# Optimization experiments

Hardware: AMD Instinct MI355X
Metric: run time of the kernel (lower is better)

Reference implementation:

```python
import jax, jax.numpy as jnp
import numpy as np

N_NODES = 50000
N_EDGES = 800000
D_IN = 256
D_HID = 256
D_OUT = 256
BN_EPS = 1e-5
NORM_EPS = 1e-12


def _glorot(key, out_dim, in_dim):
    a = np.sqrt(6.0 / (in_dim + out_dim)).astype(np.float32)
    return jax.random.uniform(key, (out_dim, in_dim), jnp.float32, -a, a)


def setup_inputs() -> dict:
    key = jax.random.key(0)
    ks = jax.random.split(key, 8)
    x = jax.random.normal(ks[0], (N_NODES, D_IN), jnp.float32)
    edge_index = jax.random.randint(ks[1], (2, N_EDGES), 0, N_NODES, dtype=jnp.int32)
    batch = jnp.zeros((N_NODES,), jnp.int32)
    return {
        "x": x,
        "W1_l": _glorot(ks[2], D_HID, D_IN),
        "b1_l": jnp.zeros((D_HID,), jnp.float32),
        "W1_r": _glorot(ks[3], D_HID, D_IN),
        "W2_l": _glorot(ks[4], D_OUT, D_HID),
        "b2_l": jnp.zeros((D_OUT,), jnp.float32),
        "W2_r": _glorot(ks[5], D_OUT, D_HID),
        "gamma1": jnp.ones((D_HID,), jnp.float32),
        "beta1": jnp.zeros((D_HID,), jnp.float32),
        "edge_index": edge_index,
        "batch": batch,
    }


def _sage_conv(x, W_l, b_l, W_r, src, dst, n_nodes):
    # PyG SAGEConv (aggr='mean'): out = lin_l(mean_j x_j) + lin_r(x)
    msgs = x[src]                                            # [E, d] gather
    s = jax.ops.segment_sum(msgs, dst, num_segments=n_nodes)  # [N, d] scatter-add
    cnt = jax.ops.segment_sum(jnp.ones((src.shape[0], 1), x.dtype), dst,
                              num_segments=n_nodes)
    agg = jnp.where(cnt > 0, s / jnp.maximum(cnt, 1.0), 0.0)
    return agg @ W_l.T + b_l + x @ W_r.T


def _batch_norm(h, gamma, beta):
    mu = jnp.mean(h, axis=0)
    var = jnp.mean((h - mu) ** 2, axis=0)  # biased, as torch train-mode BN
    return (h - mu) * jax.lax.rsqrt(var + BN_EPS) * gamma + beta


def _l2_normalize(h):
    n = jnp.linalg.norm(h, axis=-1, keepdims=True)
    return h / jnp.maximum(n, NORM_EPS)


def reference(x, W1_l, b1_l, W1_r, W2_l, b2_l, W2_r, gamma1, beta1,
              edge_index, batch):
    n = x.shape[0]
    src, dst = edge_index[0], edge_index[1]
    # layer 1: SAGEConv -> BN (train stats) -> ReLU (dropout = identity in eval)
    h = _sage_conv(x, W1_l, b1_l, W1_r, src, dst, n)
    h = jax.nn.relu(_batch_norm(h, gamma1, beta1))
    # layer 2: SAGEConv -> L2 normalize
    h = _sage_conv(h, W2_l, b2_l, W2_r, src, dst, n)
    node_emb = _l2_normalize(h)
    # global mean pool over batch ids (single graph here), then normalize
    gsum = jax.ops.segment_sum(node_emb, batch, num_segments=1)
    gcnt = jax.ops.segment_sum(jnp.ones((n, 1), node_emb.dtype), batch,
                               num_segments=1)
    graph_emb = _l2_normalize(gsum / jnp.maximum(gcnt, 1.0))
    return node_emb, graph_emb
```

## Files before the change

kernel.cpp:

```cpp
#include <hip/hip_runtime.h>
#include <math.h>

#define NN 50000
#define NE 800000
#define D  256
#define SCB 196

typedef unsigned short u16;
typedef __attribute__((ext_vector_type(8))) short short8;
typedef __attribute__((ext_vector_type(8))) unsigned short u16x8;
typedef __attribute__((ext_vector_type(4))) float f32x4;

__device__ __forceinline__ u16 f2b(float f) {
    unsigned u = __float_as_uint(f);
    return (u16)((u + 0x7FFFu + ((u >> 16) & 1u)) >> 16);
}
__device__ __forceinline__ float b2f(u16 b) {
    return __uint_as_float(((unsigned)b) << 16);
}

__device__ __forceinline__ void gl16(const u16* g, u16* l) {
    __builtin_amdgcn_global_load_lds(
        (const __attribute__((address_space(1))) void*)g,
        (__attribute__((address_space(3))) void*)l, 16, 0, 0);
}

__global__ void degree_kernel(const int* __restrict__ dst, int* __restrict__ deg) {
    int e = blockIdx.x * blockDim.x + threadIdx.x;
    if (e < NE) atomicAdd(&deg[dst[e]], 1);
}

__global__ void scanA_kernel(const int* __restrict__ deg, int* __restrict__ partial) {
    int t = threadIdx.x;
    int i = blockIdx.x * 256 + t;
    int v = (i < NN) ? deg[i] : 0;
#pragma unroll
    for (int o = 32; o; o >>= 1) v += __shfl_xor(v, o);
    __shared__ int sm[4];
    if ((t & 63) == 0) sm[t >> 6] = v;
    __syncthreads();
    if (t == 0) partial[blockIdx.x] = sm[0] + sm[1] + sm[2] + sm[3];
}

__global__ void scanB_kernel(const int* __restrict__ partial, int* __restrict__ base,
                             int* __restrict__ offs) {
    __shared__ int sm[256];
    int t = threadIdx.x;
    int v = (t < SCB) ? partial[t] : 0;
    sm[t] = v;
    __syncthreads();
    for (int off = 1; off < 256; off <<= 1) {
        int u = 0;
        if (t >= off) u = sm[t - off];
        __syncthreads();
        sm[t] += u;
        __syncthreads();
    }
    if (t < SCB) base[t] = sm[t] - v;
    if (t == 255) offs[NN] = sm[255];
}

__global__ void scanC_kernel(const int* __restrict__ deg, const int* __restrict__ base,
                             int* __restrict__ offs, int* __restrict__ cur) {
    __shared__ int sm[256];
    int t = threadIdx.x;
    int i = blockIdx.x * 256 + t;
    int v = (i < NN) ? deg[i] : 0;
    sm[t] = v;
    __syncthreads();
    for (int off = 1; off < 256; off <<= 1) {
        int u = 0;
        if (t >= off) u = sm[t - off];
        __syncthreads();
        sm[t] += u;
        __syncthreads();
    }
    int o = base[blockIdx.x] + sm[t] - v;
    if (i < NN) {
        offs[i] = o;
        cur[i] = o;
    }
}

__global__ void fill_kernel(const int* __restrict__ src, const int* __restrict__ dst,
                            int* __restrict__ cur, int* __restrict__ csr) {
    int e = blockIdx.x * blockDim.x + threadIdx.x;
    if (e < NE) {
        int pos = atomicAdd(&cur[dst[e]], 1);
        csr[pos] = src[e];
    }
}

__global__ void wconv_kernel(const float* __restrict__ W1l, const float* __restrict__ W1r,
                             const float* __restrict__ W2l, const float* __restrict__ W2r,
                             u16* __restrict__ Wcat1, u16* __restrict__ Wcat2) {
    int r = blockIdx.x;
    int j = threadIdx.x;
    Wcat1[r * 512 + j]       = f2b(W1l[r * 256 + j]);
    Wcat1[r * 512 + 256 + j] = f2b(W1r[r * 256 + j]);
    Wcat2[r * 512 + j]       = f2b(W2l[r * 256 + j]);
    Wcat2[r * 512 + 256 + j] = f2b(W2r[r * 256 + j]);
}

__global__ void xconv_kernel(const float* __restrict__ x, u16* __restrict__ Acat) {
    int idx = blockIdx.x * blockDim.x + threadIdx.x;
    int r = idx >> 6;
    int c4 = (idx & 63) * 4;
    float4 v = *(const float4*)&x[(size_t)r * 256 + c4];
    ushort4 o;
    o.x = f2b(v.x); o.y = f2b(v.y); o.z = f2b(v.z); o.w = f2b(v.w);
    *(ushort4*)&Acat[(size_t)r * 512 + 256 + c4] = o;
}

__global__ __launch_bounds__(256)
void agg_kernel(const u16* __restrict__ Acat, const int* __restrict__ csr,
                const int* __restrict__ offs, u16* __restrict__ AcatW) {
    int wid = (blockIdx.x * blockDim.x + threadIdx.x) >> 6;
    int lane = threadIdx.x & 63;
    if (wid >= NN) return;
    int beg = offs[wid];
    int end = offs[wid + 1];
    int deg = end - beg;
    int half = lane >> 5;
    int lc = (lane & 31) * 8;
    int mid = beg + ((deg + 1) >> 1);
    int e  = half ? mid : beg;
    int hi = half ? end : mid;
    float a[8] = {0.f, 0.f, 0.f, 0.f, 0.f, 0.f, 0.f, 0.f};
    for (; e + 3 < hi; e += 4) {
        int s0 = csr[e + 0];
        int s1 = csr[e + 1];
        int s2 = csr[e + 2];
        int s3 = csr[e + 3];
        u16x8 v0 = *(const u16x8*)&Acat[(size_t)s0 * 512 + 256 + lc];
        u16x8 v1 = *(const u16x8*)&Acat[(size_t)s1 * 512 + 256 + lc];
        u16x8 v2 = *(const u16x8*)&Acat[(size_t)s2 * 512 + 256 + lc];
        u16x8 v3 = *(const u16x8*)&Acat[(size_t)s3 * 512 + 256 + lc];
#pragma unroll
        for (int i = 0; i < 8; i++)
            a[i] += (b2f(v0[i]) + b2f(v1[i])) + (b2f(v2[i]) + b2f(v3[i]));
    }
    for (; e < hi; e++) {
        int s0 = csr[e];
        u16x8 v0 = *(const u16x8*)&Acat[(size_t)s0 * 512 + 256 + lc];
#pragma unroll
        for (int i = 0; i < 8; i++) a[i] += b2f(v0[i]);
    }
#pragma unroll
    for (int i = 0; i < 8; i++) a[i] += __shfl_xor(a[i], 32);
    float sc = (deg > 0) ? 1.0f / (float)deg : 0.0f;
    if (half == 0) {
        u16x8 o;
#pragma unroll
        for (int i = 0; i < 8; i++) o[i] = f2b(a[i] * sc);
        *(u16x8*)&AcatW[(size_t)wid * 512 + lc] = o;
    }
}

template<int BF16_OUT>
__global__ __launch_bounds__(256)
void mfma_gemm_kernel(const u16* __restrict__ A, const u16* __restrict__ W,
                      const float* __restrict__ bias, void* __restrict__ Cout) {
    __shared__ u16 As[4][128 * 32];
    __shared__ u16 Bs[4][128 * 32];
    const int tid = threadIdx.x;
    const int l = tid & 63;
    const int wid = tid >> 6;
    const int wr = wid >> 1, wc = wid & 1;
    const int row0 = blockIdx.x * 128;
    const int col0 = blockIdx.y * 128;

    const u16* aptr[2];
    const u16* bptr[2];
#pragma unroll
    for (int i = 0; i < 2; i++) {
        int row = wid * 32 + i * 16 + (l >> 2);
        int kg = (l & 3) ^ ((row >> 1) & 3);
        int ra = row0 + row;
        if (ra > NN - 1) ra = NN - 1;
        aptr[i] = A + (size_t)ra * 512 + kg * 8;
        bptr[i] = W + (size_t)(col0 + row) * 512 + kg * 8;
    }

    f32x4 acc[4][4] = {};

#define STAGE(b, t)                                                          \
    do {                                                                     \
        _Pragma("unroll") for (int i_ = 0; i_ < 2; i_++) {                   \
            u16* al = &As[b][(wid * 32 + i_ * 16) * 32];                     \
            u16* bl = &Bs[b][(wid * 32 + i_ * 16) * 32];                     \
            gl16(aptr[i_] + (t) * 32, al);                                   \
            gl16(bptr[i_] + (t) * 32, bl);                                   \
        }                                                                    \
    } while (0)

    STAGE(0, 0);
    STAGE(1, 1);

    const int kq = l >> 4;
    const int sw = ((l & 15) >> 1) & 3;
#pragma unroll
    for (int t = 0; t < 16; t++) {
        if (t + 2 < 16) STAGE((t + 2) & 3, t + 2);

        if (t < 14)       asm volatile("s_waitcnt vmcnt(8)" ::: "memory");
        else if (t == 14) asm volatile("s_waitcnt vmcnt(4)" ::: "memory");
        else              asm volatile("s_waitcnt vmcnt(0)" ::: "memory");
        __builtin_amdgcn_s_barrier();
        __builtin_amdgcn_sched_barrier(0);

        short8 af[4], bf[4];
#pragma unroll
        for (int m = 0; m < 4; m++) {
            int row = wr * 64 + m * 16 + (l & 15);
            af[m] = *(const short8*)&As[t & 3][row * 32 + (kq ^ sw) * 8];
        }
#pragma unroll
        for (int n = 0; n < 4; n++) {
            int row = wc * 64 + n * 16 + (l & 15);
            bf[n] = *(const short8*)&Bs[t & 3][row * 32 + (kq ^ sw) * 8];
        }
#pragma unroll
        for (int m = 0; m < 4; m++)
#pragma unroll
            for (int n = 0; n < 4; n++)
                acc[m][n] = __builtin_amdgcn_mfma_f32_16x16x32_bf16(
                    af[m], bf[n], acc[m][n], 0, 0, 0);
    }
#undef STAGE

    const int cq = l >> 4;
    const int cc = l & 15;
#pragma unroll
    for (int m = 0; m < 4; m++) {
#pragma unroll
        for (int n = 0; n < 4; n++) {
#pragma unroll
            for (int j = 0; j < 4; j++) {
                int r = row0 + wr * 64 + m * 16 + cq * 4 + j;
                int c = col0 + wc * 64 + n * 16 + cc;
                if (r < NN) {
                    float v = acc[m][n][j] + bias[c];
                    if (BF16_OUT)
                        ((u16*)Cout)[(size_t)r * 256 + c] = f2b(v);
                    else
                        ((float*)Cout)[(size_t)r * 256 + c] = v;
                }
            }
        }
    }
}

__global__ void colstats_kernel(const u16* __restrict__ h, float* __restrict__ stats) {
    int j = threadIdx.x;
    float s0 = 0.f, s1 = 0.f;
    for (int r = blockIdx.x; r < NN; r += gridDim.x) {
        float v = b2f(h[(size_t)r * 256 + j]);
        s0 += v;
        s1 += v * v;
    }
    atomicAdd(&stats[j], s0);
    atomicAdd(&stats[256 + j], s1);
}

__global__ void bnfin_kernel(const float* __restrict__ stats,
                             const float* __restrict__ gamma,
                             const float* __restrict__ beta,
                             float* __restrict__ scale,
                             float* __restrict__ shift) {
    int j = threadIdx.x;
    const float invN = 1.0f / (float)NN;
    float mu = stats[j] * invN;
    float var = stats[256 + j] * invN - mu * mu;
    float sc = gamma[j] * rsqrtf(var + 1e-5f);
    scale[j] = sc;
    shift[j] = beta[j] - mu * sc;
}

__global__ void bnrelu_kernel(const u16* __restrict__ hb,
                              const float* __restrict__ scale,
                              const float* __restrict__ shift,
                              u16* __restrict__ Acat) {
    int idx = blockIdx.x * blockDim.x + threadIdx.x;
    int r = idx >> 5;
    int c8 = (idx & 31) * 8;
    u16x8 v = *(const u16x8*)&hb[(size_t)r * 256 + c8];
    u16x8 o;
#pragma unroll
    for (int i = 0; i < 8; i++) {
        float f = b2f(v[i]) * scale[c8 + i] + shift[c8 + i];
        o[i] = f2b(fmaxf(f, 0.f));
    }
    *(u16x8*)&Acat[(size_t)r * 512 + 256 + c8] = o;
}

__global__ __launch_bounds__(512)
void l2norm_kernel(float* __restrict__ out, float* __restrict__ gsum) {
    __shared__ float sm[8 * 256];
    int wave = threadIdx.x >> 6;
    int lane = threadIdx.x & 63;
    float c0 = 0.f, c1 = 0.f, c2 = 0.f, c3 = 0.f;
    for (int r = blockIdx.x * 8 + wave; r < NN; r += gridDim.x * 8) {
        float4 v = *(float4*)&out[(size_t)r * 256 + lane * 4];
        float sq = v.x * v.x + v.y * v.y + v.z * v.z + v.w * v.w;
#pragma unroll
        for (int o = 32; o; o >>= 1) sq += __shfl_xor(sq, o);
        float invn = 1.0f / fmaxf(sqrtf(sq), 1e-12f);
        v.x *= invn; v.y *= invn; v.z *= invn; v.w *= invn;
        *(float4*)&out[(size_t)r * 256 + lane * 4] = v;
        c0 += v.x; c1 += v.y; c2 += v.z; c3 += v.w;
    }
    *(float4*)&sm[wave * 256 + lane * 4] = make_float4(c0, c1, c2, c3);
    __syncthreads();
    int t = threadIdx.x;
    if (t < 256) {
        float s = 0.f;
#pragma unroll
        for (int w = 0; w < 8; w++) s += sm[w * 256 + t];
        atomicAdd(&gsum[t], s);
    }
}

__global__ void graph_kernel(const float* __restrict__ gsum, float* __restrict__ gout) {
    __shared__ float wsum[4];
    int j = threadIdx.x;
    float v = gsum[j] * (1.0f / (float)NN);
    float sq = v * v;
#pragma unroll
    for (int o = 32; o; o >>= 1) sq += __shfl_xor(sq, o);
    if ((j & 63) == 0) wsum[j >> 6] = sq;
    __syncthreads();
    float tot = wsum[0] + wsum[1] + wsum[2] + wsum[3];
    gout[j] = v / fmaxf(sqrtf(tot), 1e-12f);
}

extern "C" void kernel_launch(void* const* d_in, const int* in_sizes, int n_in,
                              void* d_out, int out_size, void* d_ws, size_t ws_size,
                              hipStream_t stream) {
    const float* x      = (const float*)d_in[0];
    const float* W1_l   = (const float*)d_in[1];
    const float* b1_l   = (const float*)d_in[2];
    const float* W1_r   = (const float*)d_in[3];
    const float* W2_l   = (const float*)d_in[4];
    const float* b2_l   = (const float*)d_in[5];
    const float* W2_r   = (const float*)d_in[6];
    const float* gamma1 = (const float*)d_in[7];
    const float* beta1  = (const float*)d_in[8];
    const int*   eidx   = (const int*)d_in[9];
    const int* src = eidx;
    const int* dst = eidx + NE;

    char* wsb = (char*)d_ws;
    int*   deg   = (int*)(wsb + 0);
    int*   offs  = (int*)(wsb + 200000);
    int*   cur   = (int*)(wsb + 400004);
    int*   csr   = (int*)(wsb + 600004);
    int*   part  = (int*)(wsb + 3800064);
    int*   base  = (int*)(wsb + 3801088);
    float* stats = (float*)(wsb + 3802112);
    float* gsum  = (float*)(wsb + 3804160);
    float* scale = (float*)(wsb + 3805184);
    float* shift = (float*)(wsb + 3806208);
    u16*   Wcat1 = (u16*)(wsb + 3807232);
    u16*   Wcat2 = (u16*)(wsb + 4069376);
    u16*   hb    = (u16*)(wsb + 4331520);
    u16*   Acat  = (u16*)(wsb + 29931520);
    float* out   = (float*)d_out;
    float* gout  = out + (size_t)NN * 256;

    hipMemsetAsync(deg, 0, NN * sizeof(int), stream);
    hipMemsetAsync(stats, 0, 3072, stream);

    wconv_kernel<<<256, 256, 0, stream>>>(W1_l, W1_r, W2_l, W2_r, Wcat1, Wcat2);
    xconv_kernel<<<12500, 256, 0, stream>>>(x, Acat);

    degree_kernel<<<(NE + 255) / 256, 256, 0, stream>>>(dst, deg);
    scanA_kernel<<<SCB, 256, 0, stream>>>(deg, part);
    scanB_kernel<<<1, 256, 0, stream>>>(part, base, offs);
    scanC_kernel<<<SCB, 256, 0, stream>>>(deg, base, offs, cur);
    fill_kernel<<<(NE + 255) / 256, 256, 0, stream>>>(src, dst, cur, csr);

    dim3 ggrid((NN + 127) / 128, 2);

    agg_kernel<<<12500, 256, 0, stream>>>(Acat, csr, offs, Acat);
    mfma_gemm_kernel<1><<<ggrid, 256, 0, stream>>>(Acat, Wcat1, b1_l, hb);
    colstats_kernel<<<512, 256, 0, stream>>>(hb, stats);
    bnfin_kernel<<<1, 256, 0, stream>>>(stats, gamma1, beta1, scale, shift);
    bnrelu_kernel<<<6250, 256, 0, stream>>>(hb, scale, shift, Acat);

    agg_kernel<<<12500, 256, 0, stream>>>(Acat, csr, offs, Acat);
    mfma_gemm_kernel<0><<<ggrid, 256, 0, stream>>>(Acat, Wcat2, b2_l, out);

    l2norm_kernel<<<1024, 512, 0, stream>>>(out, gsum);
    graph_kernel<<<1, 256, 0, stream>>>(gsum, gout);
}
```

Baseline: 395.4 us.

## Fuse BN column stats into GEMM epilogue, vectorize CSR build, unroll aggregation

Removes the separate column-statistics pass over the hidden activations by accumulating per-column sum and sum-of-squares in the first GEMM's epilogue, reducing across lanes with shuffles and committing with atomics. The degree and CSR-fill kernels now process four edges per thread with int4 loads. The aggregation loop is unrolled to eight neighbours so more gathers are in flight. The trade-offs are more atomics from GEMM blocks and higher register pressure in aggregation. Stats are now taken on the fp32 values before bf16 rounding, which shifts numerics slightly.

```diff
diff --git a/kernel.cpp b/kernel.cpp
--- a/kernel.cpp
+++ b/kernel.cpp
@@ -26,8 +26,16 @@
 }
 
 __global__ void degree_kernel(const int* __restrict__ dst, int* __restrict__ deg) {
-    int e = blockIdx.x * blockDim.x + threadIdx.x;
-    if (e < NE) atomicAdd(&deg[dst[e]], 1);
+    int e0 = (blockIdx.x * blockDim.x + threadIdx.x) * 4;
+    if (e0 + 3 < NE) {
+        int4 d = *(const int4*)&dst[e0];
+        atomicAdd(&deg[d.x], 1);
+        atomicAdd(&deg[d.y], 1);
+        atomicAdd(&deg[d.z], 1);
+        atomicAdd(&deg[d.w], 1);
+    } else {
+        for (int e = e0; e < NE; e++) atomicAdd(&deg[dst[e]], 1);
+    }
 }
 
 __global__ void scanA_kernel(const int* __restrict__ deg, int* __restrict__ partial) {
@@ -84,10 +92,23 @@
 
 __global__ void fill_kernel(const int* __restrict__ src, const int* __restrict__ dst,
                             int* __restrict__ cur, int* __restrict__ csr) {
-    int e = blockIdx.x * blockDim.x + threadIdx.x;
-    if (e < NE) {
-        int pos = atomicAdd(&cur[dst[e]], 1);
-        csr[pos] = src[e];
+    int e0 = (blockIdx.x * blockDim.x + threadIdx.x) * 4;
+    if (e0 + 3 < NE) {
+        int4 d = *(const int4*)&dst[e0];
+        int4 s = *(const int4*)&src[e0];
+        int p0 = atomicAdd(&cur[d.x], 1);
+        int p1 = atomicAdd(&cur[d.y], 1);
+        int p2 = atomicAdd(&cur[d.z], 1);
+        int p3 = atomicAdd(&cur[d.w], 1);
+        csr[p0] = s.x;
+        csr[p1] = s.y;
+        csr[p2] = s.z;
+        csr[p3] = s.w;
+    } else {
+        for (int e = e0; e < NE; e++) {
+            int pos = atomicAdd(&cur[dst[e]], 1);
+            csr[pos] = src[e];
+        }
     }
 }
 
@@ -127,15 +148,28 @@
     int e  = half ? mid : beg;
     int hi = half ? end : mid;
     float a[8] = {0.f, 0.f, 0.f, 0.f, 0.f, 0.f, 0.f, 0.f};
-    for (; e + 3 < hi; e += 4) {
-        int s0 = csr[e + 0];
-        int s1 = csr[e + 1];
-        int s2 = csr[e + 2];
-        int s3 = csr[e + 3];
+    for (; e + 7 < hi; e += 8) {
+        int s0 = csr[e + 0], s1 = csr[e + 1], s2 = csr[e + 2], s3 = csr[e + 3];
+        int s4 = csr[e + 4], s5 = csr[e + 5], s6 = csr[e + 6], s7 = csr[e + 7];
         u16x8 v0 = *(const u16x8*)&Acat[(size_t)s0 * 512 + 256 + lc];
         u16x8 v1 = *(const u16x8*)&Acat[(size_t)s1 * 512 + 256 + lc];
         u16x8 v2 = *(const u16x8*)&Acat[(size_t)s2 * 512 + 256 + lc];
         u16x8 v3 = *(const u16x8*)&Acat[(size_t)s3 * 512 + 256 + lc];
+        u16x8 v4 = *(const u16x8*)&Acat[(size_t)s4 * 512 + 256 + lc];
+        u16x8 v5 = *(const u16x8*)&Acat[(size_t)s5 * 512 + 256 + lc];
+        u16x8 v6 = *(const u16x8*)&Acat[(size_t)s6 * 512 + 256 + lc];
+        u16x8 v7 = *(const u16x8*)&Acat[(size_t)s7 * 512 + 256 + lc];
+#pragma unroll
+        for (int i = 0; i < 8; i++)
+            a[i] += ((b2f(v0[i]) + b2f(v1[i])) + (b2f(v2[i]) + b2f(v3[i]))) +
+                    ((b2f(v4[i]) + b2f(v5[i])) + (b2f(v6[i]) + b2f(v7[i])));
+    }
+    for (; e + 3 < hi; e += 4) {
+        int s0 = csr[e + 0], s1 = csr[e + 1], s2 = csr[e + 2], s3 = csr[e + 3];
+        u16x8 v0 = *(const u16x8*)&Acat[(size_t)s0 * 512 + 256 + lc];
+        u16x8 v1 = *(const u16x8*)&Acat[(size_t)s1 * 512 + 256 + lc];
+        u16x8 v2 = *(const u16x8*)&Acat[(size_t)s2 * 512 + 256 + lc];
+        u16x8 v3 = *(const u16x8*)&Acat[(size_t)s3 * 512 + 256 + lc];
 #pragma unroll
         for (int i = 0; i < 8; i++)
             a[i] += (b2f(v0[i]) + b2f(v1[i])) + (b2f(v2[i]) + b2f(v3[i]));
@@ -157,10 +191,11 @@
     }
 }
 
-template<int BF16_OUT>
+template<int BF16_OUT, int STATS>
 __global__ __launch_bounds__(256)
 void mfma_gemm_kernel(const u16* __restrict__ A, const u16* __restrict__ W,
-                      const float* __restrict__ bias, void* __restrict__ Cout) {
+                      const float* __restrict__ bias, void* __restrict__ Cout,
+                      float* __restrict__ stats) {
     __shared__ u16 As[4][128 * 32];
     __shared__ u16 Bs[4][128 * 32];
     const int tid = threadIdx.x;
@@ -232,35 +267,33 @@
     const int cq = l >> 4;
     const int cc = l & 15;
 #pragma unroll
-    for (int m = 0; m < 4; m++) {
-#pragma unroll
-        for (int n = 0; n < 4; n++) {
+    for (int n = 0; n < 4; n++) {
+        int c = col0 + wc * 64 + n * 16 + cc;
+        float t0 = 0.f, t1 = 0.f;
+#pragma unroll
+        for (int m = 0; m < 4; m++) {
 #pragma unroll
             for (int j = 0; j < 4; j++) {
                 int r = row0 + wr * 64 + m * 16 + cq * 4 + j;
-                int c = col0 + wc * 64 + n * 16 + cc;
                 if (r < NN) {
                     float v = acc[m][n][j] + bias[c];
                     if (BF16_OUT)
                         ((u16*)Cout)[(size_t)r * 256 + c] = f2b(v);
                     else
                         ((float*)Cout)[(size_t)r * 256 + c] = v;
+                    if (STATS) { t0 += v; t1 += v * v; }
                 }
             }
         }
-    }
-}
-
-__global__ void colstats_kernel(const u16* __restrict__ h, float* __restrict__ stats) {
-    int j = threadIdx.x;
-    float s0 = 0.f, s1 = 0.f;
-    for (int r = blockIdx.x; r < NN; r += gridDim.x) {
-        float v = b2f(h[(size_t)r * 256 + j]);
-        s0 += v;
-        s1 += v * v;
-    }
-    atomicAdd(&stats[j], s0);
-    atomicAdd(&stats[256 + j], s1);
+        if (STATS) {
+            t0 += __shfl_xor(t0, 16); t1 += __shfl_xor(t1, 16);
+            t0 += __shfl_xor(t0, 32); t1 += __shfl_xor(t1, 32);
+            if (cq == 0) {
+                atomicAdd(&stats[c], t0);
+                atomicAdd(&stats[256 + c], t1);
+            }
+        }
+    }
 }
 
 __global__ void bnfin_kernel(const float* __restrict__ stats,
@@ -374,22 +407,21 @@
     wconv_kernel<<<256, 256, 0, stream>>>(W1_l, W1_r, W2_l, W2_r, Wcat1, Wcat2);
     xconv_kernel<<<12500, 256, 0, stream>>>(x, Acat);
 
-    degree_kernel<<<(NE + 255) / 256, 256, 0, stream>>>(dst, deg);
+    degree_kernel<<<(NE / 4 + 255) / 256, 256, 0, stream>>>(dst, deg);
     scanA_kernel<<<SCB, 256, 0, stream>>>(deg, part);
     scanB_kernel<<<1, 256, 0, stream>>>(part, base, offs);
     scanC_kernel<<<SCB, 256, 0, stream>>>(deg, base, offs, cur);
-    fill_kernel<<<(NE + 255) / 256, 256, 0, stream>>>(src, dst, cur, csr);
+    fill_kernel<<<(NE / 4 + 255) / 256, 256, 0, stream>>>(src, dst, cur, csr);
 
     dim3 ggrid((NN + 127) / 128, 2);
 
     agg_kernel<<<12500, 256, 0, stream>>>(Acat, csr, offs, Acat);
-    mfma_gemm_kernel<1><<<ggrid, 256, 0, stream>>>(Acat, Wcat1, b1_l, hb);
-    colstats_kernel<<<512, 256, 0, stream>>>(hb, stats);
+    mfma_gemm_kernel<1, 1><<<ggrid, 256, 0, stream>>>(Acat, Wcat1, b1_l, hb, stats);
     bnfin_kernel<<<1, 256, 0, stream>>>(stats, gamma1, beta1, scale, shift);
     bnrelu_kernel<<<6250, 256, 0, stream>>>(hb, scale, shift, Acat);
 
     agg_kernel<<<12500, 256, 0, stream>>>(Acat, csr, offs, Acat);
-    mfma_gemm_kernel<0><<<ggrid, 256, 0, stream>>>(Acat, Wcat2, b2_l, out);
+    mfma_gemm_kernel<0, 0><<<ggrid, 256, 0, stream>>>(Acat, Wcat2, b2_l, out, stats);
 
     l2norm_kernel<<<1024, 512, 0, stream>>>(out, gsum);
     graph_kernel<<<1, 256, 0, stream>>>(gsum, gout);
```

Result: faster. 376.9 us (-4.7%).
